# Optimization experiments

Measured on AMD Instinct MI355X. Metric: run time of the kernel, lower is better.

The kernel has to match this reference:

```python
import jax, jax.numpy as jnp
import numpy as np

K = 3
STRIDE = 1
PAD = 1


def _bilinear_gather(x, ys, xs):
    # x: [B,C,H,W]; ys, xs: [B,n,Ho,Wo] float sample positions. Zero padding outside.
    B, C, H, W = x.shape
    y0 = jnp.floor(ys)
    x0 = jnp.floor(xs)
    wy1 = ys - y0
    wx1 = xs - x0
    x_flat = x.reshape(B, C, H * W)

    def corner(yc, xc, w):
        valid = (yc >= 0) & (yc <= H - 1) & (xc >= 0) & (xc <= W - 1)
        yi = jnp.clip(yc, 0, H - 1).astype(jnp.int32)
        xi = jnp.clip(xc, 0, W - 1).astype(jnp.int32)
        idx = (yi * W + xi).reshape(B, 1, -1)
        vals = jnp.take_along_axis(x_flat, jnp.broadcast_to(idx, (B, C, idx.shape[-1])), axis=2)
        vals = vals.reshape(B, C, *ys.shape[1:])  # [B,C,n,Ho,Wo]
        return vals * (w * valid)[:, None]

    return (corner(y0, x0, (1 - wy1) * (1 - wx1))
            + corner(y0, x0 + 1, (1 - wy1) * wx1)
            + corner(y0 + 1, x0, wy1 * (1 - wx1))
            + corner(y0 + 1, x0 + 1, wy1 * wx1))


def setup_inputs() -> dict:
    key = jax.random.key(0)
    k1, k2, k3, k4 = jax.random.split(key, 4)
    B, Cin, Cout, H, W = 16, 128, 128, 64, 64
    n = K * K
    x = jax.random.normal(k1, (B, Cin, H, W), dtype=jnp.float32)
    # main deform-conv weight (kaiming-ish scale) and bias
    fan_in = Cin * n
    weight = jax.random.normal(k2, (Cout, Cin, K, K), dtype=jnp.float32) * np.float32(np.sqrt(2.0 / fan_in))
    bias = jnp.zeros((Cout,), dtype=jnp.float32)
    # offset/mask predicting conv (small init so offsets are modest)
    off_w = jax.random.normal(k3, (3 * n, Cin, K, K), dtype=jnp.float32) * np.float32(0.01)
    off_b = jax.random.normal(k4, (3 * n,), dtype=jnp.float32) * np.float32(0.01)
    return {"x": x, "weight": weight, "bias": bias, "off_w": off_w, "off_b": off_b}


def reference(x, weight, bias, off_w, off_b):
    B, Cin, H, W = x.shape
    Cout = weight.shape[0]
    n = K * K
    Ho = (H + 2 * PAD - K) // STRIDE + 1
    Wo = (W + 2 * PAD - K) // STRIDE + 1

    # offset / mask prediction conv
    out = jax.lax.conv_general_dilated(
        x, off_w, window_strides=(STRIDE, STRIDE), padding=((PAD, PAD), (PAD, PAD)),
        dimension_numbers=("NCHW", "OIHW", "NCHW"))
    out = out + off_b[None, :, None, None]  # [B, 3n, Ho, Wo]
    offset = out[:, :2 * n].reshape(B, n, 2, Ho, Wo)  # per-tap (dy, dx)
    mask = jax.nn.sigmoid(out[:, 2 * n:])  # [B, n, Ho, Wo]

    # base sampling grid per kernel tap
    t = jnp.arange(n)
    py = (t // K).astype(jnp.float32)[:, None] + (jnp.arange(Ho) * STRIDE - PAD).astype(jnp.float32)[None, :]  # [n,Ho]
    px = (t % K).astype(jnp.float32)[:, None] + (jnp.arange(Wo) * STRIDE - PAD).astype(jnp.float32)[None, :]   # [n,Wo]
    ys = py[None, :, :, None] + offset[:, :, 0]  # [B,n,Ho,Wo]
    xs = px[None, :, None, :] + offset[:, :, 1]

    sampled = _bilinear_gather(x, ys, xs)            # [B,C,n,Ho,Wo]
    sampled = sampled * mask[:, None]                # modulated (DCNv2)
    w = weight.reshape(Cout, Cin, n)
    y = jnp.einsum("bcnhw,ocn->bohw", sampled, w)
    return y + bias[None, :, None, None]
```

## Files before the change

### kernel.cpp

```cpp
#include <hip/hip_runtime.h>
#include <hip/hip_fp16.h>


typedef unsigned int u32;
typedef __attribute__((ext_vector_type(8))) _Float16 f16x8;
typedef __attribute__((ext_vector_type(4))) float f32x4;

union U16 { uint4 u; f16x8 h; };
union H2U { __half2 h2; u32 u; };

static __device__ __forceinline__ u32 pkh(float a, float b) {
    H2U c; c.h2 = __float22half2_rn(make_float2(a, b)); return c.u;
}
static __device__ __forceinline__ u32 h1(float f) {
    return (u32)__half_as_ushort(__float2half_rn(f));
}
static __device__ __forceinline__ u32 hfma2u(u32 a, u32 w, u32 acc) {
    H2U x, y, z; x.u = a; y.u = w; z.u = acc;
    z.h2 = __hfma2(x.h2, y.h2, z.h2); return z.u;
}
static __device__ __forceinline__ u32 hmul2u(u32 a, u32 w) {
    H2U x, y; x.u = a; y.u = w;
    y.h2 = __hmul2(x.h2, y.h2); return y.u;
}

#define B_   16
#define HW_  4096
#define CU_  64

__global__ __launch_bounds__(256) void k_transpose(const float* __restrict__ x,
                                                   u32* __restrict__ xtu) {
    __shared__ float tile[32][129];
    int blk = blockIdx.x, t = threadIdx.x;
    int b = blk >> 7, hw0 = (blk & 127) << 5;
    int hwl = t & 31, cg = t >> 5;
    const float* src = x + (size_t)b * 128 * HW_ + hw0 + hwl;
#pragma unroll
    for (int i = 0; i < 16; ++i) { int c = cg + (i << 3); tile[hwl][c] = src[(size_t)c * HW_]; }
    __syncthreads();
    u32* dst = xtu + ((size_t)b * HW_ + hw0) * CU_;
    int u = t & 63, hq = t >> 6;
#pragma unroll
    for (int j = 0; j < 8; ++j) {
        int hw = (hq << 3) + j;
        dst[(size_t)hw * CU_ + u] = pkh(tile[hw][2 * u], tile[hw][2 * u + 1]);
    }
}

__global__ __launch_bounds__(256) void k_prep(const float* __restrict__ weight,
                                              const float* __restrict__ off_w,
                                              uint4* __restrict__ wtv,
                                              u32* __restrict__ woffu) {
    int idx = blockIdx.x * 256 + threadIdx.x;
    if (idx < 18432) {
        int l = idx & 63, og = (idx >> 6) & 7, ks = (idx >> 9) & 3, n = idx >> 11;
        int o = og * 16 + (l & 15);
        int c0 = ks * 32 + (l >> 4) * 8;
        u32 r[4];
#pragma unroll
        for (int q = 0; q < 4; ++q) {
            int c = c0 + 2 * q;
            r[q] = pkh(weight[((size_t)(o * 128 + c)) * 9 + n],
                       weight[((size_t)(o * 128 + c + 1)) * 9 + n]);
        }
        wtv[idx] = make_uint4(r[0], r[1], r[2], r[3]);
    } else {
        int k = idx - 18432;
        int o = k / 576, r = k % 576;
        int tap = r / 64, cu = r % 64, c = cu * 2;
        u32 v = 0u;
        if (o < 27) {
            float a = off_w[((size_t)(o * 128 + c)) * 9 + tap];
            float b = off_w[((size_t)(o * 128 + c + 1)) * 9 + tap];
            v = pkh(a, b);
        }
        woffu[k] = v;
    }
}

__global__ __launch_bounds__(256) void k_offconv(const u32* __restrict__ xtu,
                                                 const u32* __restrict__ woffu,
                                                 const float* __restrict__ off_b,
                                                 float* __restrict__ offout) {
    __shared__ __align__(16) u32 S[3][64][64];
    int blk = ((blockIdx.x & 7) << 7) + (blockIdx.x >> 3);
    int t = threadIdx.x;
    int b = blk >> 6, ho = blk & 63;
    const u32* xb = xtu + (size_t)b * HW_ * CU_;
    const uint4 z4 = {0u, 0u, 0u, 0u};
#pragma unroll
    for (int i = 0; i < 12; ++i) {
        int li = t + (i << 8);
        int r = li >> 10, rem = li & 1023;
        int px = rem >> 4, ch = rem & 15;
        int yy = ho + r - 1;
        uint4 v = ((unsigned)yy < 64u) ? *(const uint4*)(xb + ((yy << 6) + px) * CU_ + (ch << 2)) : z4;
        *(uint4*)&S[r][px][(ch ^ (px & 7)) << 2] = v;
    }
    __syncthreads();
    int lane = t & 63, w = t >> 6, l15 = lane & 15, lhi = lane >> 4;
    int ob = w >> 1, pb0 = (w & 1) << 1;
    f32x4 acc[2];
    acc[0] = (f32x4){0.f, 0.f, 0.f, 0.f};
    acc[1] = (f32x4){0.f, 0.f, 0.f, 0.f};
#pragma unroll 1
    for (int tap = 0; tap < 9; ++tap) {
        int ky = tap / 3, kx = tap % 3;
        int yy = ho + ky - 1;
        if ((unsigned)yy >= 64u) continue;
        U16 af[4];
#pragma unroll
        for (int ks = 0; ks < 4; ++ks)
            af[ks].u = *(const uint4*)(woffu + (size_t)(ob * 16 + l15) * 576
                                       + tap * 64 + ks * 16 + lhi * 4);
#pragma unroll
        for (int pp = 0; pp < 2; ++pp) {
            int pr = ((pb0 + pp) << 4) + l15;
            int pxs = pr + kx - 1;
            bool v = (unsigned)pxs < 64u;
            int pxc = v ? pxs : 0;
#pragma unroll
            for (int ks = 0; ks < 4; ++ks) {
                U16 sf;
                sf.u = v ? *(const uint4*)&S[ky][pxc][((ks * 4 + lhi) ^ (pxc & 7)) << 2] : z4;
                acc[pp] = __builtin_amdgcn_mfma_f32_16x16x32_f16(af[ks].h, sf.h, acc[pp], 0, 0, 0);
            }
        }
    }
    float* dst = offout + (size_t)b * 27 * HW_ + (ho << 6);
#pragma unroll
    for (int pp = 0; pp < 2; ++pp)
#pragma unroll
        for (int r = 0; r < 4; ++r) {
            int o = ob * 16 + lhi * 4 + r;
            if (o < 27) {
                float s = acc[pp][r] + off_b[o];
                if (o >= 18) s = 1.f / (1.f + __expf(-s));
                dst[(size_t)o * HW_ + ((pb0 + pp) << 4) + l15] = s;
            }
        }
}

__global__ __launch_bounds__(256) void k_params(const float* __restrict__ offout,
                                                uint4* __restrict__ params) {
    int g = blockIdx.x * 256 + threadIdx.x;
    int wo = g & 63, r = g >> 6;
    int tap = r % 9, bho = r / 9;
    int ho = bho & 63, b = bho >> 6;
    const float* ob_ = offout + (size_t)b * 27 * HW_ + ho * 64 + wo;
    float dy = ob_[(size_t)(2 * tap) * HW_];
    float dx = ob_[(size_t)(2 * tap + 1) * HW_];
    float m  = ob_[(size_t)(18 + tap) * HW_];
    float ys = (float)(ho + tap / 3 - 1) + dy;
    float xs = (float)(wo + tap % 3 - 1) + dx;
    float y0f = floorf(ys), x0f = floorf(xs);
    float fy = ys - y0f, fx = xs - x0f;
    int y0 = (int)y0f, x0 = (int)x0f;
    bool vy0 = (unsigned)y0 < 64u, vy1 = (unsigned)(y0 + 1) < 64u;
    bool vx0 = (unsigned)x0 < 64u, vx1 = (unsigned)(x0 + 1) < 64u;
    u32 h00 = h1((vy0 && vx0) ? (1.f - fy) * (1.f - fx) * m : 0.f);
    u32 h01 = h1((vy0 && vx1) ? (1.f - fy) * fx * m : 0.f);
    u32 h10 = h1((vy1 && vx0) ? fy * (1.f - fx) * m : 0.f);
    u32 h11 = h1((vy1 && vx1) ? fy * fx * m : 0.f);
    int y0c = min(max(y0, 0), 63), y1c = min(max(y0 + 1, 0), 63);
    int x0c = min(max(x0, 0), 63), x1c = min(max(x0 + 1, 0), 63);
    u32 a00 = ((u32)y0c << 14) + ((u32)x0c << 8);
    u32 a11 = ((u32)y1c << 14) + ((u32)x1c << 8);
    params[g] = make_uint4(h00 | (h01 << 16), h10 | (h11 << 16), a00, a11);
}

__global__ __launch_bounds__(256, 3) void k_fused(const u32* __restrict__ xtu,
                                                  const uint4* __restrict__ wtv,
                                                  const u32* __restrict__ paramsU,
                                                  const float* __restrict__ bias,
                                                  float* __restrict__ out) {
    __shared__ __align__(16) u32 S[2][64][68];
    __shared__ __align__(16) u32 PRM[2][256];
    int blk = ((blockIdx.x & 7) << 7) + (blockIdx.x >> 3);
    int t = threadIdx.x;
    int b = blk >> 6, ho = blk & 63;
    int w = t >> 6, lane = t & 63, l15 = lane & 15, lhi = lane >> 4;
    int o0 = w * 32;
    int lane4 = lane << 2;
    int wbase = w << 6;

    f32x4 acc[2][4];
#pragma unroll
    for (int ob = 0; ob < 2; ++ob)
#pragma unroll
        for (int pb = 0; pb < 4; ++pb) acc[ob][pb] = (f32x4){0.f, 0.f, 0.f, 0.f};

    const char* xbb = (const char*)(xtu + (size_t)b * HW_ * CU_);
    int pbase = ((b << 6) + ho) * 9;
    const u32* pU = paramsU + (size_t)pbase * 256 + wbase + lane;

    u32 ld[16][4];

#define ISSUE_G(NB)                                                          \
    _Pragma("unroll") for (int j = 0; j < 16; ++j) {                         \
        uint2 av = *(const uint2*)&PRM[NB][wbase + (j << 2) + 2];            \
        u32 a00 = av.x, a11 = av.y;                                          \
        u32 a01 = (a00 & ~0x3FFFu) | (a11 & 0x3FFFu);                        \
        u32 a10 = (a11 & ~0x3FFFu) | (a00 & 0x3FFFu);                        \
        ld[j][0] = *(const u32*)(xbb + a00 + lane4);                         \
        ld[j][1] = *(const u32*)(xbb + a01 + lane4);                         \
        ld[j][2] = *(const u32*)(xbb + a10 + lane4);                         \
        ld[j][3] = *(const u32*)(xbb + a11 + lane4);                         \
    }

    {
        u32 p0 = pU[0];
        u32 p1 = pU[256];
        PRM[0][wbase + lane] = p0;
        PRM[1][wbase + lane] = p1;
    }
    ISSUE_G(0);

#pragma unroll 1
    for (int n = 0; n < 9; ++n) {
        int buf = n & 1;
        u32 pr = 0u;
        if (n < 7) pr = pU[(size_t)(n + 2) * 256];
#pragma unroll
        for (int j = 0; j < 16; ++j) {
            uint2 wv = *(const uint2*)&PRM[buf][wbase + (j << 2)];
            u32 lo  = wv.x & 0xFFFFu; u32 w00p = lo  | (lo  << 16);
            u32 hi  = wv.x >> 16;     u32 w01p = hi  | (hi  << 16);
            u32 lo2 = wv.y & 0xFFFFu; u32 w10p = lo2 | (lo2 << 16);
            u32 hi2 = wv.y >> 16;     u32 w11p = hi2 | (hi2 << 16);
            u32 r = hfma2u(ld[j][3], w11p, hfma2u(ld[j][2], w10p,
                    hfma2u(ld[j][1], w01p, hmul2u(ld[j][0], w00p))));
            S[buf][(w << 4) + j][lane] = r;
        }
        U16 wf[2][4];
#pragma unroll
        for (int ob = 0; ob < 2; ++ob)
#pragma unroll
            for (int ks = 0; ks < 4; ++ks)
                wf[ob][ks].u = wtv[(((n << 2) + ks) * 8 + (w << 1) + ob) * 64 + lane];
        if (n < 7) PRM[buf][wbase + lane] = pr;
        if (n < 8) { ISSUE_G((n + 1) & 1); }
        asm volatile("s_waitcnt lgkmcnt(0)" ::: "memory");
        __builtin_amdgcn_sched_barrier(0);
        __builtin_amdgcn_s_barrier();
        __builtin_amdgcn_sched_barrier(0);
#pragma unroll
        for (int ks = 0; ks < 4; ++ks) {
            U16 sf[4];
#pragma unroll
            for (int pb = 0; pb < 4; ++pb)
                sf[pb].u = *(const uint4*)&S[buf][pb * 16 + l15][(ks * 4 + lhi) << 2];
#pragma unroll
            for (int ob = 0; ob < 2; ++ob)
#pragma unroll
                for (int pb = 0; pb < 4; ++pb)
                    acc[ob][pb] = __builtin_amdgcn_mfma_f32_16x16x32_f16(
                        wf[ob][ks].h, sf[pb].h, acc[ob][pb], 0, 0, 0);
        }
    }
#undef ISSUE_G
    float* ob_base = out + (size_t)b * 128 * HW_ + ho * 64;
#pragma unroll
    for (int ob = 0; ob < 2; ++ob)
#pragma unroll
        for (int r = 0; r < 4; ++r) {
            int o = o0 + ob * 16 + lhi * 4 + r;
            float bv = bias[o];
#pragma unroll
            for (int pb = 0; pb < 4; ++pb)
                ob_base[(size_t)o * HW_ + pb * 16 + l15] = acc[ob][pb][r] + bv;
        }
}

extern "C" void kernel_launch(void* const* d_in, const int* in_sizes, int n_in,
                              void* d_out, int out_size, void* d_ws, size_t ws_size,
                              hipStream_t stream) {
    const float* x      = (const float*)d_in[0];
    const float* weight = (const float*)d_in[1];
    const float* bias   = (const float*)d_in[2];
    const float* off_w  = (const float*)d_in[3];
    const float* off_b  = (const float*)d_in[4];
    float* out = (float*)d_out;

    u32*   xtu    = (u32*)d_ws;
    float* offout = (float*)(xtu + (size_t)B_ * HW_ * CU_);
    uint4* wtv    = (uint4*)(offout + (size_t)B_ * 27 * HW_);
    u32*   woffu  = (u32*)wtv + 294912;
    uint4* params = (uint4*)(woffu + 18432);

    hipLaunchKernelGGL(k_transpose, dim3(2048), dim3(256), 0, stream, x, xtu);
    hipLaunchKernelGGL(k_prep, dim3(144), dim3(256), 0, stream, weight, off_w, wtv, woffu);
    hipLaunchKernelGGL(k_offconv, dim3(1024), dim3(256), 0, stream, xtu, woffu, off_b, offout);
    hipLaunchKernelGGL(k_params, dim3(2304), dim3(256), 0, stream, offout, params);
    hipLaunchKernelGGL(k_fused, dim3(1024), dim3(256), 0, stream, xtu, wtv, (const u32*)params, bias, out);
}
```

Baseline: 109.0 us.

## Stage a 7-row input window in LDS and process two output rows per block

The fused deformable-conv kernel now copies a 7-row slab of the channel-last input (rows ho0-2..ho0+4) into shared memory and takes bilinear corners from LDS when the whole wave's samples fall inside that window. Otherwise it falls back to global gathers. Each 512-thread block now covers two output rows, which halves the grid, and k_params packs the corner coordinates plus an in-window flag into one word. The aim is to replace scattered global/L2 gathers with LDS reads. The cost is a large LDS footprint (about 150KB) that allows one block per CU, an upfront slab load with no overlap, and the loss of the software-pipelined prefetch of gathers.

```diff
diff --git a/kernel.cpp b/kernel.cpp
--- a/kernel.cpp
+++ b/kernel.cpp
@@ -144,9 +144,12 @@
 __global__ __launch_bounds__(256) void k_params(const float* __restrict__ offout,
                                                 uint4* __restrict__ params) {
     int g = blockIdx.x * 256 + threadIdx.x;
-    int wo = g & 63, r = g >> 6;
-    int tap = r % 9, bho = r / 9;
-    int ho = bho & 63, b = bho >> 6;
+    int local = g & 127;
+    int tmp = g >> 7;
+    int tap = tmp % 9, brp = tmp / 9;
+    int rp = brp & 31, b = brp >> 5;
+    int ho = (rp << 1) + (local >> 6), wo = local & 63;
+    int ho0 = rp << 1;
     const float* ob_ = offout + (size_t)b * 27 * HW_ + ho * 64 + wo;
     float dy = ob_[(size_t)(2 * tap) * HW_];
     float dx = ob_[(size_t)(2 * tap + 1) * HW_];
@@ -164,25 +167,27 @@
     u32 h11 = h1((vy1 && vx1) ? fy * fx * m : 0.f);
     int y0c = min(max(y0, 0), 63), y1c = min(max(y0 + 1, 0), 63);
     int x0c = min(max(x0, 0), 63), x1c = min(max(x0 + 1, 0), 63);
-    u32 a00 = ((u32)y0c << 14) + ((u32)x0c << 8);
-    u32 a11 = ((u32)y1c << 14) + ((u32)x1c << 8);
-    params[g] = make_uint4(h00 | (h01 << 16), h10 | (h11 << 16), a00, a11);
-}
-
-__global__ __launch_bounds__(256, 3) void k_fused(const u32* __restrict__ xtu,
+    u32 inb = (y0c >= ho0 - 2 && y1c <= ho0 + 4) ? 1u : 0u;
+    u32 C = (u32)y0c | ((u32)x0c << 6) | ((u32)y1c << 12) | ((u32)x1c << 18) | (inb << 24);
+    params[g] = make_uint4(h00 | (h01 << 16), h10 | (h11 << 16), C, 0u);
+}
+
+__global__ __launch_bounds__(512, 1) void k_fused(const u32* __restrict__ xtu,
                                                   const uint4* __restrict__ wtv,
                                                   const u32* __restrict__ paramsU,
                                                   const float* __restrict__ bias,
                                                   float* __restrict__ out) {
-    __shared__ __align__(16) u32 S[2][64][68];
-    __shared__ __align__(16) u32 PRM[2][256];
-    int blk = ((blockIdx.x & 7) << 7) + (blockIdx.x >> 3);
+    __shared__ __align__(16) u32 XB[7 * 4096];
+    __shared__ __align__(16) u32 S[128][68];
+    __shared__ __align__(16) u32 PRM[2][512];
+    int raw = blockIdx.x;
+    int blk = ((raw & 7) << 6) + (raw >> 3);
     int t = threadIdx.x;
-    int b = blk >> 6, ho = blk & 63;
+    int b = blk >> 5, rp = blk & 31, ho0 = rp << 1;
     int w = t >> 6, lane = t & 63, l15 = lane & 15, lhi = lane >> 4;
-    int o0 = w * 32;
+    int q = w >> 1, g = w & 1;
+    int o0 = q * 32;
     int lane4 = lane << 2;
-    int wbase = w << 6;
 
     f32x4 acc[2][4];
 #pragma unroll
@@ -190,56 +195,65 @@
 #pragma unroll
         for (int pb = 0; pb < 4; ++pb) acc[ob][pb] = (f32x4){0.f, 0.f, 0.f, 0.f};
 
-    const char* xbb = (const char*)(xtu + (size_t)b * HW_ * CU_);
-    int pbase = ((b << 6) + ho) * 9;
-    const u32* pU = paramsU + (size_t)pbase * 256 + wbase + lane;
-
-    u32 ld[16][4];
-
-#define ISSUE_G(NB)                                                          \
-    _Pragma("unroll") for (int j = 0; j < 16; ++j) {                         \
-        uint2 av = *(const uint2*)&PRM[NB][wbase + (j << 2) + 2];            \
-        u32 a00 = av.x, a11 = av.y;                                          \
-        u32 a01 = (a00 & ~0x3FFFu) | (a11 & 0x3FFFu);                        \
-        u32 a10 = (a11 & ~0x3FFFu) | (a00 & 0x3FFFu);                        \
-        ld[j][0] = *(const u32*)(xbb + a00 + lane4);                         \
-        ld[j][1] = *(const u32*)(xbb + a01 + lane4);                         \
-        ld[j][2] = *(const u32*)(xbb + a10 + lane4);                         \
-        ld[j][3] = *(const u32*)(xbb + a11 + lane4);                         \
-    }
-
-    {
-        u32 p0 = pU[0];
-        u32 p1 = pU[256];
-        PRM[0][wbase + lane] = p0;
-        PRM[1][wbase + lane] = p1;
-    }
-    ISSUE_G(0);
+    const u32* xb = xtu + (size_t)b * HW_ * CU_;
+    const char* xbb = (const char*)xb;
+    const u32* pU = paramsU + ((size_t)(b * 32 + rp) * 9) * 512 + t;
+
+#pragma unroll
+    for (int i = 0; i < 14; ++i) {
+        int idx = t + (i << 9);
+        int r = idx >> 10, c4 = idx & 1023;
+        int phys = min(max(ho0 - 2 + r, 0), 63);
+        ((uint4*)XB)[idx] = *(const uint4*)(xb + ((size_t)phys << 12) + (c4 << 2));
+    }
+    PRM[0][t] = pU[0];
+    __syncthreads();
 
 #pragma unroll 1
     for (int n = 0; n < 9; ++n) {
         int buf = n & 1;
-        u32 pr = 0u;
-        if (n < 7) pr = pU[(size_t)(n + 2) * 256];
+        u32 prn = 0u;
+        if (n < 8) prn = pU[(size_t)(n + 1) * 512];
+        if (n > 0) {
+            __builtin_amdgcn_sched_barrier(0);
+            __builtin_amdgcn_s_barrier();
+            __builtin_amdgcn_sched_barrier(0);
+        }
 #pragma unroll
         for (int j = 0; j < 16; ++j) {
-            uint2 wv = *(const uint2*)&PRM[buf][wbase + (j << 2)];
-            u32 lo  = wv.x & 0xFFFFu; u32 w00p = lo  | (lo  << 16);
-            u32 hi  = wv.x >> 16;     u32 w01p = hi  | (hi  << 16);
-            u32 lo2 = wv.y & 0xFFFFu; u32 w10p = lo2 | (lo2 << 16);
-            u32 hi2 = wv.y >> 16;     u32 w11p = hi2 | (hi2 << 16);
-            u32 r = hfma2u(ld[j][3], w11p, hfma2u(ld[j][2], w10p,
-                    hfma2u(ld[j][1], w01p, hmul2u(ld[j][0], w00p))));
-            S[buf][(w << 4) + j][lane] = r;
+            int p = (w << 4) + j;
+            uint4 P = *(const uint4*)&PRM[buf][p << 2];
+            u32 wA = P.x, wB = P.y, C = P.z;
+            u32 w00p = (wA & 0xFFFFu) | (wA << 16);
+            u32 w01p = (wA >> 16) | (wA & 0xFFFF0000u);
+            u32 w10p = (wB & 0xFFFFu) | (wB << 16);
+            u32 w11p = (wB >> 16) | (wB & 0xFFFF0000u);
+            int y0c = C & 63, x0c = (C >> 6) & 63;
+            int y1c = (C >> 12) & 63, x1c = (C >> 18) & 63;
+            u32 v0, v1, v2, v3;
+            if (__builtin_amdgcn_readfirstlane((C >> 24) & 1)) {
+                int s0 = (y0c - ho0 + 2) << 12, s1 = (y1c - ho0 + 2) << 12;
+                v0 = XB[s0 + (x0c << 6) + lane];
+                v1 = XB[s0 + (x1c << 6) + lane];
+                v2 = XB[s1 + (x0c << 6) + lane];
+                v3 = XB[s1 + (x1c << 6) + lane];
+            } else {
+                v0 = *(const u32*)(xbb + (y0c << 14) + (x0c << 8) + lane4);
+                v1 = *(const u32*)(xbb + (y0c << 14) + (x1c << 8) + lane4);
+                v2 = *(const u32*)(xbb + (y1c << 14) + (x0c << 8) + lane4);
+                v3 = *(const u32*)(xbb + (y1c << 14) + (x1c << 8) + lane4);
+            }
+            u32 r = hfma2u(v3, w11p, hfma2u(v2, w10p,
+                    hfma2u(v1, w01p, hmul2u(v0, w00p))));
+            S[p][lane] = r;
         }
         U16 wf[2][4];
 #pragma unroll
         for (int ob = 0; ob < 2; ++ob)
 #pragma unroll
             for (int ks = 0; ks < 4; ++ks)
-                wf[ob][ks].u = wtv[(((n << 2) + ks) * 8 + (w << 1) + ob) * 64 + lane];
-        if (n < 7) PRM[buf][wbase + lane] = pr;
-        if (n < 8) { ISSUE_G((n + 1) & 1); }
+                wf[ob][ks].u = wtv[(((n << 2) + ks) * 8 + (q << 1) + ob) * 64 + lane];
+        if (n < 8) PRM[buf ^ 1][t] = prn;
         asm volatile("s_waitcnt lgkmcnt(0)" ::: "memory");
         __builtin_amdgcn_sched_barrier(0);
         __builtin_amdgcn_s_barrier();
@@ -249,7 +263,7 @@
             U16 sf[4];
 #pragma unroll
             for (int pb = 0; pb < 4; ++pb)
-                sf[pb].u = *(const uint4*)&S[buf][pb * 16 + l15][(ks * 4 + lhi) << 2];
+                sf[pb].u = *(const uint4*)&S[(g << 6) + pb * 16 + l15][(ks * 4 + lhi) << 2];
 #pragma unroll
             for (int ob = 0; ob < 2; ++ob)
 #pragma unroll
@@ -258,8 +272,7 @@
                         wf[ob][ks].h, sf[pb].h, acc[ob][pb], 0, 0, 0);
         }
     }
-#undef ISSUE_G
-    float* ob_base = out + (size_t)b * 128 * HW_ + ho * 64;
+    float* ob_base = out + (size_t)b * 128 * HW_ + (ho0 + g) * 64;
 #pragma unroll
     for (int ob = 0; ob < 2; ++ob)
 #pragma unroll
@@ -292,5 +305,5 @@
     hipLaunchKernelGGL(k_prep, dim3(144), dim3(256), 0, stream, weight, off_w, wtv, woffu);
     hipLaunchKernelGGL(k_offconv, dim3(1024), dim3(256), 0, stream, xtu, woffu, off_b, offout);
     hipLaunchKernelGGL(k_params, dim3(2304), dim3(256), 0, stream, offout, params);
-    hipLaunchKernelGGL(k_fused, dim3(1024), dim3(256), 0, stream, xtu, wtv, (const u32*)params, bias, out);
-}
+    hipLaunchKernelGGL(k_fused, dim3(512), dim3(512), 0, stream, xtu, wtv, (const u32*)params, bias, out);
+}
```

New measurement: 134.4 us. 1.23x slower.
